# Performance work log

Hardware: AMD Instinct MI355X
Metric: run time of the kernel (lower is better)

## Reference

```python
import jax, jax.numpy as jnp
import numpy as np

LOCAL = (1, 2, 2, 2)
NUM_HEADS = 8


def conv4d(x, w, b):
    # x: (B, L, C, D, H, W); w: (Cout, Cin, 3) temporal conv, 'same' padding on L.
    L = x.shape[1]
    xp = jnp.pad(x, ((0, 0), (1, 1), (0, 0), (0, 0), (0, 0), (0, 0)))
    y = (jnp.einsum('blcdhw,oc->blodhw', xp[:, 0:L], w[:, :, 0])
         + jnp.einsum('blcdhw,oc->blodhw', xp[:, 1:L + 1], w[:, :, 1])
         + jnp.einsum('blcdhw,oc->blodhw', xp[:, 2:L + 2], w[:, :, 2]))
    return y + b[None, None, :, None, None, None]


def to_windows(x):
    # (B, L, C, D, H, W) -> (B, nlw, heads, ws, hd)
    B, L, C, D, H, W = x.shape
    l0, l1, l2, l3 = LOCAL
    nl, nd, nh, nw = L // l0, D // l1, H // l2, W // l3
    x = jnp.transpose(x, (0, 2, 1, 3, 4, 5))  # B C L D H W
    x = x.reshape(B, C, nl, l0, nd, l1, nh, l2, nw, l3)
    x = jnp.transpose(x, (0, 2, 4, 6, 8, 3, 5, 7, 9, 1))  # B nl nd nh nw l0 l1 l2 l3 C
    nlw, ws = nl * nd * nh * nw, l0 * l1 * l2 * l3
    x = x.reshape(B, nlw, ws, NUM_HEADS, C // NUM_HEADS)
    return jnp.transpose(x, (0, 1, 3, 2, 4))


def from_windows(y, shape):
    # (B, nlw, heads, ws, hd) -> (B, L, C, D, H, W)
    B, L, C, D, H, W = shape
    l0, l1, l2, l3 = LOCAL
    nl, nd, nh, nw = L // l0, D // l1, H // l2, W // l3
    y = jnp.transpose(y, (0, 1, 3, 2, 4)).reshape(B, nl, nd, nh, nw, l0, l1, l2, l3, C)
    y = jnp.transpose(y, (0, 9, 1, 5, 2, 6, 3, 7, 4, 8)).reshape(B, C, L, D, H, W)
    return jnp.transpose(y, (0, 2, 1, 3, 4, 5))


def window_attn(q, k, v, scale):
    attn = jax.nn.softmax(jnp.einsum('bnhqd,bnhkd->bnhqk', q, k) * scale, axis=-1)
    return jnp.einsum('bnhqk,bnhkd->bnhqd', attn, v)


def tlg_forward(x, wq, bq, wk, bk, wv, bv, wp, bp):
    B, L, C, D, H, W = x.shape
    scale = (C // NUM_HEADS) ** (-0.5)
    half_shape = (B, L // 2, C, D, H, W)
    xs, xe = x[:, :L // 2], x[:, L // 2:]
    # start-queries attend to end keys/values
    qs = to_windows(conv4d(xs, wq, bq))
    ke = to_windows(conv4d(xe, wk, bk))
    ve = to_windows(conv4d(xe, wv, bv))
    yse = from_windows(window_attn(qs, ke, ve, scale), half_shape)
    yse = conv4d(yse, wp, bp)
    # end-queries attend to start keys/values
    qe = to_windows(conv4d(xe, wq, bq))
    ks = to_windows(conv4d(xs, wk, bk))
    vs = to_windows(conv4d(xs, wv, bv))
    yes = from_windows(window_attn(qe, ks, vs, scale), half_shape)
    yes = conv4d(yes, wp, bp)
    return jnp.concatenate([yse, yes], axis=1)


def setup_inputs() -> dict:
    key = jax.random.key(0)
    ks = jax.random.split(key, 10)
    C = 128
    wscale = 1.0 / np.sqrt(C * 3)
    x = jax.random.normal(ks[0], (2, 8, C, 16, 32, 32), dtype=jnp.float32)
    def w(k):
        return jax.random.normal(k, (C, C, 3), dtype=jnp.float32) * wscale
    def b(k):
        return jax.random.normal(k, (C,), dtype=jnp.float32) * 0.01
    return {
        'x': x,
        'wq': w(ks[1]), 'bq': b(ks[2]),
        'wk': w(ks[3]), 'bk': b(ks[4]),
        'wv': w(ks[5]), 'bv': b(ks[6]),
        'wp': w(ks[7]), 'bp': b(ks[8]),
    }


def reference(x, wq, bq, wk, bk, wv, bv, wp, bp):
    return tlg_forward(x, wq, bq, wk, bk, wv, bv, wp, bp)
```

## Files before the change

kernel.cpp:

```cpp
#include <hip/hip_runtime.h>

typedef __attribute__((ext_vector_type(8))) short short8;
typedef __attribute__((ext_vector_type(4))) float v4f;

#define C_CH 128
#define S_SP 16384
#define NSLICE 16
#define KTOT 384

__device__ inline float bf2f(unsigned short u) {
  union { unsigned int i; float f; } v; v.i = ((unsigned int)u) << 16; return v.f;
}
__device__ inline unsigned short f2bf(float f) {
  union { float f; unsigned int i; } v; v.f = f;
  unsigned int u = v.i;
  return (unsigned short)((u + 0x7FFFu + ((u >> 16) & 1u)) >> 16);
}

__device__ inline void gload_lds16(const unsigned short* g, unsigned short* l) {
  __builtin_amdgcn_global_load_lds(
      (const __attribute__((address_space(1))) void*)g,
      (__attribute__((address_space(3))) void*)l, 16, 0, 0);
}

__global__ __launch_bounds__(256) void repack_kernel(
    const float* __restrict__ wq, const float* __restrict__ wk,
    const float* __restrict__ wv, const float* __restrict__ wp,
    const float* __restrict__ bq, const float* __restrict__ bk,
    const float* __restrict__ bv, const float* __restrict__ bp,
    unsigned short* __restrict__ Wr, float* __restrict__ biasf)
{
  int i = blockIdx.x * 256 + threadIdx.x;
  const int WN = 4 * 49152;
  if (i < WN) {
    int m = i / 49152;
    int r = i % 49152;
    int o = r / 384, k = r % 384;
    int t = k >> 7, c = k & 127;
    const float* w = (m == 0) ? wq : (m == 1) ? wk : (m == 2) ? wv : wp;
    Wr[i] = f2bf(w[o * 384 + c * 3 + t]);
  } else if (i < WN + 512) {
    int j = i - WN;
    int m = j >> 7, o = j & 127;
    const float* bb = (m == 0) ? bq : (m == 1) ? bk : (m == 2) ? bv : bp;
    biasf[j] = bb[o];
  }
}

__global__ __launch_bounds__(256) void transpose_f2b_kernel(
    const float* __restrict__ in, unsigned short* __restrict__ out,
    int R, int C)
{
  __shared__ unsigned short t[64][72];
  int tid = threadIdx.x;
  size_t slice = blockIdx.z;
  const float* ip = in + slice * (size_t)R * C;
  unsigned short* op = out + slice * (size_t)R * C;
  int c0 = blockIdx.x * 64, r0 = blockIdx.y * 64;
#pragma unroll
  for (int p = 0; p < 4; ++p) {
    int id = tid + p * 256;
    int row = id >> 4, col = (id & 15) * 4;
    float4 v = *(const float4*)(ip + (size_t)(r0 + row) * C + c0 + col);
    t[row][col + 0] = f2bf(v.x);
    t[row][col + 1] = f2bf(v.y);
    t[row][col + 2] = f2bf(v.z);
    t[row][col + 3] = f2bf(v.w);
  }
  __syncthreads();
#pragma unroll
  for (int p = 0; p < 2; ++p) {
    int id = tid + p * 256;
    int crow = id >> 3, rcol = (id & 7) * 8;
    uint4 v;
    v.x = (unsigned)t[rcol + 0][crow] | ((unsigned)t[rcol + 1][crow] << 16);
    v.y = (unsigned)t[rcol + 2][crow] | ((unsigned)t[rcol + 3][crow] << 16);
    v.z = (unsigned)t[rcol + 4][crow] | ((unsigned)t[rcol + 5][crow] << 16);
    v.w = (unsigned)t[rcol + 6][crow] | ((unsigned)t[rcol + 7][crow] << 16);
    *(uint4*)(op + (size_t)(c0 + crow) * R + r0 + rcol) = v;
  }
}

__global__ __launch_bounds__(256) void transpose_b2f_kernel(
    const unsigned short* __restrict__ in, float* __restrict__ out,
    int R, int C)
{
  __shared__ unsigned short t[64][72];
  int tid = threadIdx.x;
  size_t slice = blockIdx.z;
  const unsigned short* ip = in + slice * (size_t)R * C;
  float* op = out + slice * (size_t)R * C;
  int c0 = blockIdx.x * 64, r0 = blockIdx.y * 64;
#pragma unroll
  for (int p = 0; p < 2; ++p) {
    int id = tid + p * 256;
    int row = id >> 3, col = (id & 7) * 8;
    uint4 v = *(const uint4*)(ip + (size_t)(r0 + row) * C + c0 + col);
    *(uint4*)(&t[row][col]) = v;
  }
  __syncthreads();
#pragma unroll
  for (int p = 0; p < 4; ++p) {
    int id = tid + p * 256;
    int crow = id >> 4, rcol = (id & 15) * 4;
    float4 v;
    v.x = bf2f(t[rcol + 0][crow]);
    v.y = bf2f(t[rcol + 1][crow]);
    v.z = bf2f(t[rcol + 2][crow]);
    v.w = bf2f(t[rcol + 3][crow]);
    *(float4*)(op + (size_t)(c0 + crow) * R + r0 + rcol) = v;
  }
}

__global__ __launch_bounds__(256, 3) void conv_mfma_kernel(
    const unsigned short* __restrict__ inT,
    const unsigned short* __restrict__ Wr_all,
    const float* __restrict__ bias_all,
    unsigned short* __restrict__ outT_all)
{
  __shared__ unsigned short Blds[3][128 * 64];

  int z = blockIdx.z;
  const unsigned short* Wr = Wr_all + (size_t)z * 49152;
  const float* bias = bias_all + z * 128;
  unsigned short* outT = outT_all + (size_t)z * NSLICE * S_SP * C_CH;

  int tid = threadIdx.x;
  int s0 = blockIdx.x * 128;
  int slice = blockIdx.y;
  int b = slice >> 3, l = slice & 7;
  int lh = l & 3;
  int t_lo = (lh == 0) ? 1 : 0;
  int t_hi = (lh == 3) ? 1 : 2;
  int lo = t_lo * 2, hi = t_hi * 2 + 1;

  int w = tid >> 6, lane = tid & 63;
  int quad = lane >> 4, l15 = lane & 15;
  int srow_i = lane >> 3;
  int scs = (lane & 7) ^ srow_i;

  v4f acc[2][8];
#pragma unroll
  for (int i = 0; i < 2; ++i)
#pragma unroll
    for (int j = 0; j < 8; ++j)
      acc[i][j] = (v4f){0.f, 0.f, 0.f, 0.f};

  short8 af0[4], af1[4], af2[4];

#define STAGE(ap, bsel) do {                                                   \
    int t_ = (ap) >> 1;                                                        \
    const unsigned short* gb_ =                                                \
        inT + ((size_t)(b * 8 + l - 1 + t_) * S_SP + s0) * C_CH +              \
        ((ap) & 1) * 64;                                                       \
    _Pragma("unroll")                                                          \
    for (int q_ = 0; q_ < 4; ++q_)                                             \
      gload_lds16(gb_ + (size_t)((w * 4 + q_) * 8 + srow_i) * C_CH + scs * 8,  \
                  &Blds[bsel][(w * 4 + q_) * 512]);                            \
  } while (0)

#define AFLOAD(ap, set) do {                                                   \
    _Pragma("unroll")                                                          \
    for (int i_ = 0; i_ < 2; ++i_)                                             \
      _Pragma("unroll")                                                        \
      for (int ks_ = 0; ks_ < 2; ++ks_)                                        \
        set[i_ * 2 + ks_] = *(const short8*)(                                  \
            Wr + (size_t)(w * 32 + i_ * 16 + l15) * KTOT +                     \
            (ap) * 64 + ks_ * 32 + quad * 8);                                  \
  } while (0)

  if (lo == 0) {
    STAGE(0, 0); AFLOAD(0, af0);
    __builtin_amdgcn_sched_barrier(0);
    STAGE(1, 1); AFLOAD(1, af1);
  } else {
    STAGE(2, 2); AFLOAD(2, af2);
    __builtin_amdgcn_sched_barrier(0);
    STAGE(3, 0); AFLOAD(3, af0);
  }

#define PHASE(ap, CURSET, NXTSET)                                              \
  if ((ap) >= lo && (ap) <= hi) {                                              \
    if ((ap) == hi) { asm volatile("s_waitcnt vmcnt(0)" ::: "memory"); }       \
    else            { asm volatile("s_waitcnt vmcnt(8)" ::: "memory"); }       \
    __builtin_amdgcn_s_barrier();                                              \
    if ((ap) + 2 <= hi) { STAGE((ap) + 2, ((ap) + 2) % 3);                     \
                          AFLOAD((ap) + 2, NXTSET); }                          \
    const unsigned short* Bp_ = &Blds[(ap) % 3][0];                            \
    _Pragma("unroll")                                                          \
    for (int ks = 0; ks < 2; ++ks) {                                           \
      _Pragma("unroll")                                                        \
      for (int jg = 0; jg < 2; ++jg) {                                         \
        short8 bfr[4];                                                         \
        _Pragma("unroll")                                                      \
        for (int j4 = 0; j4 < 4; ++j4)                                         \
          bfr[j4] = *(const short8*)(                                          \
              Bp_ + ((jg * 4 + j4) * 16 + l15) * 64 +                          \
              (((ks * 4 + quad) ^ (l15 & 7)) * 8));                            \
        _Pragma("unroll")                                                      \
        for (int i = 0; i < 2; ++i)                                            \
          _Pragma("unroll")                                                    \
          for (int j4 = 0; j4 < 4; ++j4)                                       \
            acc[i][jg * 4 + j4] = __builtin_amdgcn_mfma_f32_16x16x32_bf16(     \
                CURSET[i * 2 + ks], bfr[j4], acc[i][jg * 4 + j4], 0, 0, 0);    \
      }                                                                        \
    }                                                                          \
  }

  PHASE(0, af0, af2)
  PHASE(1, af1, af0)
  PHASE(2, af2, af1)
  PHASE(3, af0, af2)
  PHASE(4, af1, af0)
  PHASE(5, af2, af0)

#undef PHASE
#undef AFLOAD
#undef STAGE

#pragma unroll
  for (int i = 0; i < 2; ++i) {
    int obase = w * 32 + i * 16 + quad * 4;
    float4 bb = *(const float4*)(bias + obase);
#pragma unroll
    for (int j = 0; j < 8; ++j) {
      int s = s0 + j * 16 + l15;
      float f0 = acc[i][j].x + bb.x;
      float f1 = acc[i][j].y + bb.y;
      float f2 = acc[i][j].z + bb.z;
      float f3 = acc[i][j].w + bb.w;
      uint2 st;
      st.x = (unsigned)f2bf(f0) | ((unsigned)f2bf(f1) << 16);
      st.y = (unsigned)f2bf(f2) | ((unsigned)f2bf(f3) << 16);
      *(uint2*)(outT + ((size_t)slice * S_SP + s) * C_CH + obase) = st;
    }
  }
}

__device__ inline void load16(const unsigned short* p, float* f) {
  uint4 a = *(const uint4*)p;
  uint4 c = *(const uint4*)(p + 8);
  unsigned v[8] = {a.x, a.y, a.z, a.w, c.x, c.y, c.z, c.w};
#pragma unroll
  for (int i = 0; i < 8; ++i) {
    f[2 * i] = bf2f((unsigned short)(v[i] & 0xffffu));
    f[2 * i + 1] = bf2f((unsigned short)(v[i] >> 16));
  }
}

__global__ __launch_bounds__(256) void attn_kernel(
    const unsigned short* __restrict__ QT,
    const unsigned short* __restrict__ KT,
    const unsigned short* __restrict__ VT,
    unsigned short* __restrict__ YT)
{
  int tid = threadIdx.x;
  int wave = tid >> 6, lane = tid & 63;
  int dir = wave & 1;
  int win = blockIdx.x * 2 + (wave >> 1);
  int by = blockIdx.y;
  int b = by >> 2, l0 = by & 3;
  int head = lane >> 3, qi = lane & 7;
  int d0 = win >> 8, h0 = (win >> 4) & 15, w0 = win & 15;
  int lq = l0 + dir * 4;
  int lk = l0 + 4 - dir * 4;
  int sE[8];
#pragma unroll
  for (int e = 0; e < 8; ++e)
    sE[e] = (2 * d0 + (e >> 2)) * 1024 + (2 * h0 + ((e >> 1) & 1)) * 32 + (2 * w0 + (e & 1));

  size_t qbase = ((size_t)(b * 8 + lq) * S_SP + sE[qi]) * C_CH + head * 16;
  size_t kslice = (size_t)(b * 8 + lk) * S_SP;
  float q[16];
  load16(QT + qbase, q);

  float lg[8];
#pragma unroll
  for (int j = 0; j < 8; ++j) {
    float kk[16];
    load16(KT + (kslice + sE[j]) * C_CH + head * 16, kk);
    float d = 0.f;
#pragma unroll
    for (int x = 0; x < 16; ++x) d += q[x] * kk[x];
    lg[j] = d * 0.25f;
  }
  float m = lg[0];
#pragma unroll
  for (int j = 1; j < 8; ++j) m = fmaxf(m, lg[j]);
  float p[8], sum = 0.f;
#pragma unroll
  for (int j = 0; j < 8; ++j) { p[j] = __expf(lg[j] - m); sum += p[j]; }
  float inv = 1.0f / sum;

  float y[16];
#pragma unroll
  for (int x = 0; x < 16; ++x) y[x] = 0.f;
#pragma unroll
  for (int j = 0; j < 8; ++j) {
    float vv[16];
    load16(VT + (kslice + sE[j]) * C_CH + head * 16, vv);
    float pj = p[j] * inv;
#pragma unroll
    for (int x = 0; x < 16; ++x) y[x] += pj * vv[x];
  }
  uint4 o0, o1;
  o0.x = (unsigned)f2bf(y[0]) | ((unsigned)f2bf(y[1]) << 16);
  o0.y = (unsigned)f2bf(y[2]) | ((unsigned)f2bf(y[3]) << 16);
  o0.z = (unsigned)f2bf(y[4]) | ((unsigned)f2bf(y[5]) << 16);
  o0.w = (unsigned)f2bf(y[6]) | ((unsigned)f2bf(y[7]) << 16);
  o1.x = (unsigned)f2bf(y[8]) | ((unsigned)f2bf(y[9]) << 16);
  o1.y = (unsigned)f2bf(y[10]) | ((unsigned)f2bf(y[11]) << 16);
  o1.z = (unsigned)f2bf(y[12]) | ((unsigned)f2bf(y[13]) << 16);
  o1.w = (unsigned)f2bf(y[14]) | ((unsigned)f2bf(y[15]) << 16);
  *(uint4*)(YT + qbase) = o0;
  *(uint4*)(YT + qbase + 8) = o1;
}

extern "C" void kernel_launch(void* const* d_in, const int* in_sizes, int n_in,
                              void* d_out, int out_size, void* d_ws, size_t ws_size,
                              hipStream_t stream) {
  const float* x  = (const float*)d_in[0];
  const float* wq = (const float*)d_in[1];
  const float* bq = (const float*)d_in[2];
  const float* wk = (const float*)d_in[3];
  const float* bk = (const float*)d_in[4];
  const float* wv = (const float*)d_in[5];
  const float* bv = (const float*)d_in[6];
  const float* wp = (const float*)d_in[7];
  const float* bp = (const float*)d_in[8];

  char* ws = (char*)d_ws;
  unsigned short* Wr = (unsigned short*)ws;
  float* biasf = (float*)(ws + 393216);
  size_t off = 395264;
  const size_t TENB = (size_t)NSLICE * S_SP * C_CH * 2;
  unsigned short* xT = (unsigned short*)(ws + off); off += TENB;
  unsigned short* QT = (unsigned short*)(ws + off); off += TENB;
  unsigned short* KT = (unsigned short*)(ws + off); off += TENB;
  unsigned short* VT = (unsigned short*)(ws + off); off += TENB;
  unsigned short* YT = xT;
  unsigned short* OT = QT;

  hipLaunchKernelGGL(repack_kernel, dim3(770), dim3(256), 0, stream,
                     wq, wk, wv, wp, bq, bk, bv, bp, Wr, biasf);
  hipLaunchKernelGGL(transpose_f2b_kernel, dim3(256, 2, 16), dim3(256), 0, stream,
                     x, xT, 128, 16384);
  hipLaunchKernelGGL(conv_mfma_kernel, dim3(128, 16, 3), dim3(256), 0, stream,
                     xT, Wr, biasf, QT);
  hipLaunchKernelGGL(attn_kernel, dim3(1024, 8), dim3(256), 0, stream,
                     QT, KT, VT, YT);
  hipLaunchKernelGGL(conv_mfma_kernel, dim3(128, 16, 1), dim3(256), 0, stream,
                     YT, Wr + 3 * 49152, biasf + 384, OT);
  hipLaunchKernelGGL(transpose_b2f_kernel, dim3(2, 256, 16), dim3(256), 0, stream,
                     OT, (float*)d_out, 16384, 128);
}
```

Before: 490.6 us.

## Fuse QKV convs into one pass and fold output transpose into projection conv

```diff
diff --git a/kernel.cpp b/kernel.cpp
--- a/kernel.cpp
+++ b/kernel.cpp
@@ -81,49 +81,144 @@
   }
 }
 
-__global__ __launch_bounds__(256) void transpose_b2f_kernel(
-    const unsigned short* __restrict__ in, float* __restrict__ out,
-    int R, int C)
-{
-  __shared__ unsigned short t[64][72];
-  int tid = threadIdx.x;
-  size_t slice = blockIdx.z;
-  const unsigned short* ip = in + slice * (size_t)R * C;
-  float* op = out + slice * (size_t)R * C;
-  int c0 = blockIdx.x * 64, r0 = blockIdx.y * 64;
-#pragma unroll
-  for (int p = 0; p < 2; ++p) {
-    int id = tid + p * 256;
-    int row = id >> 3, col = (id & 7) * 8;
-    uint4 v = *(const uint4*)(ip + (size_t)(r0 + row) * C + c0 + col);
-    *(uint4*)(&t[row][col]) = v;
-  }
-  __syncthreads();
-#pragma unroll
-  for (int p = 0; p < 4; ++p) {
-    int id = tid + p * 256;
-    int crow = id >> 4, rcol = (id & 15) * 4;
-    float4 v;
-    v.x = bf2f(t[rcol + 0][crow]);
-    v.y = bf2f(t[rcol + 1][crow]);
-    v.z = bf2f(t[rcol + 2][crow]);
-    v.w = bf2f(t[rcol + 3][crow]);
-    *(float4*)(op + (size_t)(c0 + crow) * R + r0 + rcol) = v;
-  }
-}
-
-__global__ __launch_bounds__(256, 3) void conv_mfma_kernel(
+__global__ __launch_bounds__(256, 2) void conv_qkv_kernel(
     const unsigned short* __restrict__ inT,
     const unsigned short* __restrict__ Wr_all,
     const float* __restrict__ bias_all,
-    unsigned short* __restrict__ outT_all)
+    unsigned short* __restrict__ outQ)
 {
-  __shared__ unsigned short Blds[3][128 * 64];
-
-  int z = blockIdx.z;
-  const unsigned short* Wr = Wr_all + (size_t)z * 49152;
-  const float* bias = bias_all + z * 128;
-  unsigned short* outT = outT_all + (size_t)z * NSLICE * S_SP * C_CH;
+  __shared__ unsigned short Blds[3][64 * 64];
+
+  int tid = threadIdx.x;
+  int s0 = blockIdx.x * 64;
+  int slice = blockIdx.y;
+  int b = slice >> 3, l = slice & 7;
+  int lh = l & 3;
+  int t_lo = (lh == 0) ? 1 : 0;
+  int t_hi = (lh == 3) ? 1 : 2;
+  int lo = t_lo * 2, hi = t_hi * 2 + 1;
+
+  int w = tid >> 6, lane = tid & 63;
+  int quad = lane >> 4, l15 = lane & 15;
+  int srow_i = lane >> 3;
+  int scs = (lane & 7) ^ srow_i;
+
+  v4f acc[3][2][4];
+#pragma unroll
+  for (int z_ = 0; z_ < 3; ++z_)
+#pragma unroll
+    for (int i = 0; i < 2; ++i)
+#pragma unroll
+      for (int j = 0; j < 4; ++j)
+        acc[z_][i][j] = (v4f){0.f, 0.f, 0.f, 0.f};
+
+  short8 afA[12], afB[12];
+
+#define STAGE(ap, bsel) do {                                                   \
+    int t_ = (ap) >> 1;                                                        \
+    const unsigned short* gb_ =                                                \
+        inT + ((size_t)(b * 8 + l - 1 + t_) * S_SP + s0) * C_CH +              \
+        ((ap) & 1) * 64;                                                       \
+    _Pragma("unroll")                                                          \
+    for (int q_ = 0; q_ < 2; ++q_)                                             \
+      gload_lds16(gb_ + (size_t)((w * 2 + q_) * 8 + srow_i) * C_CH + scs * 8,  \
+                  &Blds[bsel][(w * 2 + q_) * 512]);                            \
+  } while (0)
+
+#define AFLOAD(ap, set) do {                                                   \
+    _Pragma("unroll")                                                          \
+    for (int z_ = 0; z_ < 3; ++z_)                                             \
+      _Pragma("unroll")                                                        \
+      for (int i_ = 0; i_ < 2; ++i_)                                           \
+        _Pragma("unroll")                                                      \
+        for (int ks_ = 0; ks_ < 2; ++ks_)                                      \
+          set[z_ * 4 + i_ * 2 + ks_] = *(const short8*)(                       \
+              Wr_all + (size_t)z_ * 49152 +                                    \
+              (size_t)(w * 32 + i_ * 16 + l15) * KTOT +                        \
+              (ap) * 64 + ks_ * 32 + quad * 8);                                \
+  } while (0)
+
+  {
+    int ap0 = lo;
+    STAGE(ap0, ap0 % 3);
+    __builtin_amdgcn_sched_barrier(0);
+    AFLOAD(ap0, afA);
+    __builtin_amdgcn_sched_barrier(0);
+    STAGE(ap0 + 1, (ap0 + 1) % 3);
+    __builtin_amdgcn_sched_barrier(0);
+  }
+
+#define PHASE(ap, CUR, NXT)                                                    \
+  if ((ap) >= lo && (ap) <= hi) {                                              \
+    if ((ap) == hi) { asm volatile("s_waitcnt vmcnt(0)" ::: "memory"); }       \
+    else            { asm volatile("s_waitcnt vmcnt(2)" ::: "memory"); }       \
+    __builtin_amdgcn_s_barrier();                                              \
+    if ((ap) + 1 <= hi) { AFLOAD((ap) + 1, NXT);                               \
+                          __builtin_amdgcn_sched_barrier(0); }                 \
+    if ((ap) + 2 <= hi) { STAGE((ap) + 2, ((ap) + 2) % 3);                     \
+                          __builtin_amdgcn_sched_barrier(0); }                 \
+    const unsigned short* Bp_ = &Blds[(ap) % 3][0];                            \
+    _Pragma("unroll")                                                          \
+    for (int ks = 0; ks < 2; ++ks) {                                           \
+      short8 bfr[4];                                                           \
+      _Pragma("unroll")                                                        \
+      for (int j4 = 0; j4 < 4; ++j4)                                           \
+        bfr[j4] = *(const short8*)(                                            \
+            Bp_ + (j4 * 16 + l15) * 64 +                                       \
+            (((ks * 4 + quad) ^ (l15 & 7)) * 8));                              \
+      _Pragma("unroll")                                                        \
+      for (int z_ = 0; z_ < 3; ++z_)                                           \
+        _Pragma("unroll")                                                      \
+        for (int i = 0; i < 2; ++i)                                            \
+          _Pragma("unroll")                                                    \
+          for (int j4 = 0; j4 < 4; ++j4)                                       \
+            acc[z_][i][j4] = __builtin_amdgcn_mfma_f32_16x16x32_bf16(          \
+                CUR[z_ * 4 + i * 2 + ks], bfr[j4], acc[z_][i][j4], 0, 0, 0);   \
+    }                                                                          \
+  }
+
+  PHASE(0, afA, afB)
+  PHASE(1, afB, afA)
+  PHASE(2, afA, afB)
+  PHASE(3, afB, afA)
+  PHASE(4, afA, afB)
+  PHASE(5, afB, afA)
+
+#undef PHASE
+#undef AFLOAD
+#undef STAGE
+
+#pragma unroll
+  for (int z_ = 0; z_ < 3; ++z_) {
+    unsigned short* outT = outQ + (size_t)z_ * ((size_t)NSLICE * S_SP * C_CH);
+    const float* bias = bias_all + z_ * 128;
+#pragma unroll
+    for (int i = 0; i < 2; ++i) {
+      int obase = w * 32 + i * 16 + quad * 4;
+      float4 bb = *(const float4*)(bias + obase);
+#pragma unroll
+      for (int j = 0; j < 4; ++j) {
+        int s = s0 + j * 16 + l15;
+        float f0 = acc[z_][i][j].x + bb.x;
+        float f1 = acc[z_][i][j].y + bb.y;
+        float f2 = acc[z_][i][j].z + bb.z;
+        float f3 = acc[z_][i][j].w + bb.w;
+        uint2 st;
+        st.x = (unsigned)f2bf(f0) | ((unsigned)f2bf(f1) << 16);
+        st.y = (unsigned)f2bf(f2) | ((unsigned)f2bf(f3) << 16);
+        *(uint2*)(outT + ((size_t)slice * S_SP + s) * C_CH + obase) = st;
+      }
+    }
+  }
+}
+
+__global__ __launch_bounds__(256, 2) void conv_proj_kernel(
+    const unsigned short* __restrict__ YT,
+    const unsigned short* __restrict__ Wp,
+    const float* __restrict__ biasp,
+    float* __restrict__ dout)
+{
+  __shared__ unsigned short Alds[3][128 * 64];
 
   int tid = threadIdx.x;
   int s0 = blockIdx.x * 128;
@@ -146,93 +241,92 @@
     for (int j = 0; j < 8; ++j)
       acc[i][j] = (v4f){0.f, 0.f, 0.f, 0.f};
 
-  short8 af0[4], af1[4], af2[4];
-
-#define STAGE(ap, bsel) do {                                                   \
+  short8 wfA[16], wfB[16];
+
+#define PSTAGE(ap, bsel) do {                                                  \
     int t_ = (ap) >> 1;                                                        \
     const unsigned short* gb_ =                                                \
-        inT + ((size_t)(b * 8 + l - 1 + t_) * S_SP + s0) * C_CH +              \
+        YT + ((size_t)(b * 8 + l - 1 + t_) * S_SP + s0) * C_CH +               \
         ((ap) & 1) * 64;                                                       \
     _Pragma("unroll")                                                          \
     for (int q_ = 0; q_ < 4; ++q_)                                             \
       gload_lds16(gb_ + (size_t)((w * 4 + q_) * 8 + srow_i) * C_CH + scs * 8,  \
-                  &Blds[bsel][(w * 4 + q_) * 512]);                            \
+                  &Alds[bsel][(w * 4 + q_) * 512]);                            \
   } while (0)
 
-#define AFLOAD(ap, set) do {                                                   \
-    _Pragma("unroll")                                                          \
-    for (int i_ = 0; i_ < 2; ++i_)                                             \
+#define WLOAD(ap, set) do {                                                    \
+    _Pragma("unroll")                                                          \
+    for (int j_ = 0; j_ < 8; ++j_)                                             \
       _Pragma("unroll")                                                        \
       for (int ks_ = 0; ks_ < 2; ++ks_)                                        \
-        set[i_ * 2 + ks_] = *(const short8*)(                                  \
-            Wr + (size_t)(w * 32 + i_ * 16 + l15) * KTOT +                     \
+        set[j_ * 2 + ks_] = *(const short8*)(                                  \
+            Wp + (size_t)(j_ * 16 + l15) * KTOT +                              \
             (ap) * 64 + ks_ * 32 + quad * 8);                                  \
   } while (0)
 
-  if (lo == 0) {
-    STAGE(0, 0); AFLOAD(0, af0);
-    __builtin_amdgcn_sched_barrier(0);
-    STAGE(1, 1); AFLOAD(1, af1);
-  } else {
-    STAGE(2, 2); AFLOAD(2, af2);
-    __builtin_amdgcn_sched_barrier(0);
-    STAGE(3, 0); AFLOAD(3, af0);
-  }
-
-#define PHASE(ap, CURSET, NXTSET)                                              \
+  {
+    int ap0 = lo;
+    PSTAGE(ap0, ap0 % 3);
+    __builtin_amdgcn_sched_barrier(0);
+    WLOAD(ap0, wfA);
+    __builtin_amdgcn_sched_barrier(0);
+    PSTAGE(ap0 + 1, (ap0 + 1) % 3);
+    __builtin_amdgcn_sched_barrier(0);
+  }
+
+#define PPHASE(ap, CUR, NXT)                                                   \
   if ((ap) >= lo && (ap) <= hi) {                                              \
     if ((ap) == hi) { asm volatile("s_waitcnt vmcnt(0)" ::: "memory"); }       \
-    else            { asm volatile("s_waitcnt vmcnt(8)" ::: "memory"); }       \
+    else            { asm volatile("s_waitcnt vmcnt(4)" ::: "memory"); }       \
     __builtin_amdgcn_s_barrier();                                              \
-    if ((ap) + 2 <= hi) { STAGE((ap) + 2, ((ap) + 2) % 3);                     \
-                          AFLOAD((ap) + 2, NXTSET); }                          \
-    const unsigned short* Bp_ = &Blds[(ap) % 3][0];                            \
+    if ((ap) + 1 <= hi) { WLOAD((ap) + 1, NXT);                                \
+                          __builtin_amdgcn_sched_barrier(0); }                 \
+    if ((ap) + 2 <= hi) { PSTAGE((ap) + 2, ((ap) + 2) % 3);                    \
+                          __builtin_amdgcn_sched_barrier(0); }                 \
+    const unsigned short* Ap_ = &Alds[(ap) % 3][0];                            \
     _Pragma("unroll")                                                          \
     for (int ks = 0; ks < 2; ++ks) {                                           \
-      _Pragma("unroll")                                                        \
-      for (int jg = 0; jg < 2; ++jg) {                                         \
-        short8 bfr[4];                                                         \
+      short8 afr[2];                                                           \
+      _Pragma("unroll")                                                        \
+      for (int i = 0; i < 2; ++i)                                              \
+        afr[i] = *(const short8*)(                                             \
+            Ap_ + (w * 32 + i * 16 + l15) * 64 +                               \
+            (((ks * 4 + quad) ^ (l15 & 7)) * 8));                              \
+      _Pragma("unroll")                                                        \
+      for (int i = 0; i < 2; ++i)                                              \
         _Pragma("unroll")                                                      \
-        for (int j4 = 0; j4 < 4; ++j4)                                         \
-          bfr[j4] = *(const short8*)(                                          \
-              Bp_ + ((jg * 4 + j4) * 16 + l15) * 64 +                          \
-              (((ks * 4 + quad) ^ (l15 & 7)) * 8));                            \
-        _Pragma("unroll")                                                      \
-        for (int i = 0; i < 2; ++i)                                            \
-          _Pragma("unroll")                                                    \
-          for (int j4 = 0; j4 < 4; ++j4)                                       \
-            acc[i][jg * 4 + j4] = __builtin_amdgcn_mfma_f32_16x16x32_bf16(     \
-                CURSET[i * 2 + ks], bfr[j4], acc[i][jg * 4 + j4], 0, 0, 0);    \
-      }                                                                        \
+        for (int j = 0; j < 8; ++j)                                            \
+          acc[i][j] = __builtin_amdgcn_mfma_f32_16x16x32_bf16(                 \
+              afr[i], CUR[j * 2 + ks], acc[i][j], 0, 0, 0);                    \
     }                                                                          \
   }
 
-  PHASE(0, af0, af2)
-  PHASE(1, af1, af0)
-  PHASE(2, af2, af1)
-  PHASE(3, af0, af2)
-  PHASE(4, af1, af0)
-  PHASE(5, af2, af0)
-
-#undef PHASE
-#undef AFLOAD
-#undef STAGE
-
+  PPHASE(0, wfA, wfB)
+  PPHASE(1, wfB, wfA)
+  PPHASE(2, wfA, wfB)
+  PPHASE(3, wfB, wfA)
+  PPHASE(4, wfA, wfB)
+  PPHASE(5, wfB, wfA)
+
+#undef PPHASE
+#undef WLOAD
+#undef PSTAGE
+
+  float bias_r[8];
+#pragma unroll
+  for (int j = 0; j < 8; ++j) bias_r[j] = biasp[j * 16 + l15];
 #pragma unroll
   for (int i = 0; i < 2; ++i) {
-    int obase = w * 32 + i * 16 + quad * 4;
-    float4 bb = *(const float4*)(bias + obase);
+    int s = s0 + w * 32 + i * 16 + quad * 4;
 #pragma unroll
     for (int j = 0; j < 8; ++j) {
-      int s = s0 + j * 16 + l15;
-      float f0 = acc[i][j].x + bb.x;
-      float f1 = acc[i][j].y + bb.y;
-      float f2 = acc[i][j].z + bb.z;
-      float f3 = acc[i][j].w + bb.w;
-      uint2 st;
-      st.x = (unsigned)f2bf(f0) | ((unsigned)f2bf(f1) << 16);
-      st.y = (unsigned)f2bf(f2) | ((unsigned)f2bf(f3) << 16);
-      *(uint2*)(outT + ((size_t)slice * S_SP + s) * C_CH + obase) = st;
+      int o = j * 16 + l15;
+      float4 v;
+      v.x = acc[i][j].x + bias_r[j];
+      v.y = acc[i][j].y + bias_r[j];
+      v.z = acc[i][j].z + bias_r[j];
+      v.w = acc[i][j].w + bias_r[j];
+      *(float4*)(dout + ((size_t)slice * 128 + o) * 16384 + s) = v;
     }
   }
 }
@@ -339,18 +433,15 @@
   unsigned short* KT = (unsigned short*)(ws + off); off += TENB;
   unsigned short* VT = (unsigned short*)(ws + off); off += TENB;
   unsigned short* YT = xT;
-  unsigned short* OT = QT;
 
   hipLaunchKernelGGL(repack_kernel, dim3(770), dim3(256), 0, stream,
                      wq, wk, wv, wp, bq, bk, bv, bp, Wr, biasf);
   hipLaunchKernelGGL(transpose_f2b_kernel, dim3(256, 2, 16), dim3(256), 0, stream,
                      x, xT, 128, 16384);
-  hipLaunchKernelGGL(conv_mfma_kernel, dim3(128, 16, 3), dim3(256), 0, stream,
+  hipLaunchKernelGGL(conv_qkv_kernel, dim3(256, 16), dim3(256), 0, stream,
                      xT, Wr, biasf, QT);
   hipLaunchKernelGGL(attn_kernel, dim3(1024, 8), dim3(256), 0, stream,
                      QT, KT, VT, YT);
-  hipLaunchKernelGGL(conv_mfma_kernel, dim3(128, 16, 1), dim3(256), 0, stream,
-                     YT, Wr + 3 * 49152, biasf + 384, OT);
-  hipLaunchKernelGGL(transpose_b2f_kernel, dim3(2, 256, 16), dim3(256), 0, stream,
-                     OT, (float*)d_out, 16384, 128);
-}
+  hipLaunchKernelGGL(conv_proj_kernel, dim3(128, 16), dim3(256), 0, stream,
+                     YT, Wr + 3 * 49152, biasf + 384, (float*)d_out);
+}
```

After: 603.0 us. 1.23x slower.
